# Kernel tuning notes

Measured on AMD Instinct MI355X. Metric: run time of the kernel, lower is better.

The kernel has to match this reference:

```python
import jax, jax.numpy as jnp
import numpy as np
import math

RES = 1024
HEADS = 16
HEAD_RES = RES // HEADS
B, S = 2, 2048


def setup_inputs() -> dict:
    key = jax.random.key(0)
    kx, kq, kk, kv = jax.random.split(key, 4)
    scale = 1.0 / math.sqrt(RES)
    return {
        "x": jax.random.normal(kx, (B, S, RES), dtype=jnp.float32),
        "Wq": jax.random.normal(kq, (RES, RES), dtype=jnp.float32) * scale,
        "Wk": jax.random.normal(kk, (RES, RES), dtype=jnp.float32) * scale,
        "Wv": jax.random.normal(kv, (RES, RES), dtype=jnp.float32) * scale,
    }


def reference(x, Wq, Wk, Wv):
    batch, seq, _ = x.shape
    # projections (torch Linear without bias: x @ W.T; here W stored as [in, out])
    def split_heads(t):
        return t.reshape(batch, seq, HEADS, HEAD_RES).transpose(0, 2, 1, 3)  # [B,H,S,D]
    q = split_heads(x @ Wq)
    k = split_heads(x @ Wk)
    v = split_heads(x @ Wv)
    scores = jnp.einsum("bhsd,bhtd->bhst", q, k) / math.sqrt(HEAD_RES)
    attn = jax.nn.softmax(scores, axis=-1)
    out = jnp.einsum("bhst,bhtd->bhsd", attn, v)  # [B,H,S,D]
    return out.transpose(0, 2, 1, 3).reshape(batch, seq, RES)
```

## Files before the change

### kernel.cpp

```cpp
#include <hip/hip_runtime.h>

typedef _Float16 f16;
typedef _Float16 half8 __attribute__((ext_vector_type(8)));
typedef float f32x4 __attribute__((ext_vector_type(4)));
typedef unsigned int u32x4 __attribute__((ext_vector_type(4)));

#define RES 1024
#define NH 16
#define HD 64
#define BATCH 2
#define SEQ 2048
#define M_ROWS (BATCH * SEQ)

__device__ __forceinline__ void gload_lds16(const void* g, void* l) {
  __builtin_amdgcn_global_load_lds(
      (const __attribute__((address_space(1))) unsigned int*)g,
      (__attribute__((address_space(3))) unsigned int*)l, 16, 0, 0);
}

__device__ __forceinline__ unsigned pk16(float a, float b) {
  auto h = __builtin_amdgcn_cvt_pkrtz(a, b);
  return __builtin_bit_cast(unsigned, h);
}

__device__ __forceinline__ void swap32(unsigned a, unsigned b, unsigned& x, unsigned& y) {
#if __has_builtin(__builtin_amdgcn_permlane32_swap)
  auto t = __builtin_amdgcn_permlane32_swap(a, b, false, false);
  x = (unsigned)t[0];
  y = (unsigned)t[1];
#else
  unsigned ax = __shfl_xor(a, 32), bx = __shfl_xor(b, 32);
  int hi = (threadIdx.x & 63) >> 5;
  x = hi ? bx : a;
  y = hi ? b : ax;
#endif
}

__device__ __forceinline__ void swap16(unsigned a, unsigned b, unsigned& x, unsigned& y) {
#if __has_builtin(__builtin_amdgcn_permlane16_swap)
  auto t = __builtin_amdgcn_permlane16_swap(a, b, false, false);
  x = (unsigned)t[0];
  y = (unsigned)t[1];
#else
  unsigned ax = __shfl_xor(a, 16), bx = __shfl_xor(b, 16);
  int q1 = ((threadIdx.x & 63) >> 4) & 1;
  x = q1 ? bx : a;
  y = q1 ? b : ax;
#endif
}

__global__ __launch_bounds__(256) void xconv_kernel(const float* __restrict__ x,
                                                    f16* __restrict__ xh) {
  int idx = blockIdx.x * 256 + threadIdx.x;
  const float4* xv = (const float4*)x;
  float4 a = xv[idx * 2];
  float4 b = xv[idx * 2 + 1];
  half8 h;
  h[0] = (f16)a.x; h[1] = (f16)a.y; h[2] = (f16)a.z; h[3] = (f16)a.w;
  h[4] = (f16)b.x; h[5] = (f16)b.y; h[6] = (f16)b.z; h[7] = (f16)b.w;
  ((half8*)xh)[idx] = h;
}

__global__ __launch_bounds__(1024) void wtrans_kernel(const float* __restrict__ Wq,
                                                      const float* __restrict__ Wk,
                                                      const float* __restrict__ Wv,
                                                      f16* __restrict__ Wt) {
  const float* W = blockIdx.z == 0 ? Wq : (blockIdx.z == 1 ? Wk : Wv);
  f16* Wo = Wt + (size_t)blockIdx.z * RES * RES;
  __shared__ float tile[32][33];
  int n = blockIdx.x * 32 + threadIdx.x;
  int k = blockIdx.y * 32 + threadIdx.y;
  tile[threadIdx.y][threadIdx.x] = W[(size_t)k * RES + n];
  __syncthreads();
  int ko = blockIdx.y * 32 + threadIdx.x;
  int no = blockIdx.x * 32 + threadIdx.y;
  Wo[(size_t)no * RES + ko] = (f16)tile[threadIdx.x][threadIdx.y];
}

__global__ __launch_bounds__(256) void proj_gemm_kernel(const f16* __restrict__ xh,
                                                        const f16* __restrict__ Wt,
                                                        f16* __restrict__ Qh,
                                                        f16* __restrict__ Kh,
                                                        f16* __restrict__ Vt) {
  int flat = blockIdx.x;
  int swz = (flat & 7) * 96 + (flat >> 3);
  int mb = swz & 31;
  int rest = swz >> 5;
  int nb = rest & 7;
  int proj = rest >> 3;
  const f16* Bt = Wt + (size_t)proj * RES * RES;
  int m0 = mb * 128;
  int n0 = nb * 128;
  __shared__ alignas(16) f16 Als[2][128 * 32];
  __shared__ alignas(16) f16 Bls[2][128 * 32];
  int t = threadIdx.x, lane = t & 63, w = t >> 6;
  int l15 = lane & 15, quad = lane >> 4;
  int wm = w >> 1, wn = w & 1;

  f32x4 zero = {0.f, 0.f, 0.f, 0.f};
  f32x4 acc[4][4];
#pragma unroll
  for (int mt = 0; mt < 4; mt++)
#pragma unroll
    for (int nt = 0; nt < 4; nt++) acc[mt][nt] = zero;

  auto stageAB = [&](int k0, int pb) {
#pragma unroll
    for (int i = 0; i < 2; i++) {
      int wl = i * 256 + w * 64;
      int linear = wl + lane;
      int row = linear >> 2;
      int kk = (linear & 3) * 8;
      gload_lds16(xh + (size_t)(m0 + row) * RES + k0 + kk, &Als[pb][wl * 8]);
      gload_lds16(Bt + (size_t)(n0 + row) * RES + k0 + kk, &Bls[pb][wl * 8]);
    }
  };

  stageAB(0, 0);

  constexpr int KSTEPS = RES / 32;
  for (int it = 0; it < KSTEPS; ++it) {
    int pb = it & 1;
    __syncthreads();

    half8 af[4], bf[4];
#pragma unroll
    for (int mt = 0; mt < 4; mt++)
      af[mt] = *(const half8*)&Als[pb][(wm * 64 + mt * 16 + l15) * 32 + quad * 8];
#pragma unroll
    for (int nt = 0; nt < 4; nt++)
      bf[nt] = *(const half8*)&Bls[pb][(wn * 64 + nt * 16 + l15) * 32 + quad * 8];

    if (it + 1 < KSTEPS) stageAB((it + 1) * 32, pb ^ 1);

#pragma unroll
    for (int mt = 0; mt < 4; mt++)
#pragma unroll
      for (int nt = 0; nt < 4; nt++)
        acc[mt][nt] = __builtin_amdgcn_mfma_f32_16x16x32_f16(af[mt], bf[nt], acc[mt][nt], 0, 0, 0);
  }

#pragma unroll
  for (int mt = 0; mt < 4; mt++) {
#pragma unroll
    for (int nt = 0; nt < 4; nt++) {
#pragma unroll
      for (int r = 0; r < 4; r++) {
        int row = m0 + wm * 64 + mt * 16 + quad * 4 + r;
        int col = n0 + wn * 64 + nt * 16 + l15;
        f16 v = (f16)acc[mt][nt][r];
        int b = row >> 11, s = row & (SEQ - 1);
        int h = col >> 6, d = col & (HD - 1);
        size_t bh = (size_t)b * NH + h;
        if (proj == 0)
          Qh[(bh * SEQ + s) * HD + d] = v;
        else if (proj == 1)
          Kh[(bh * SEQ + s) * HD + d] = v;
        else
          Vt[(bh * HD + d) * SEQ + s] = v;
      }
    }
  }
}

__global__ __launch_bounds__(128, 3) void flash_kernel(const f16* __restrict__ Qh,
                                                       const f16* __restrict__ Kh,
                                                       const f16* __restrict__ Vt,
                                                       float* __restrict__ out) {
  int L = blockIdx.x;
  int xcd = L & 7, slot = L >> 3;
  int bh = ((slot >> 5) << 3) | xcd;
  int qt = slot & 31;
  int b = bh >> 4, h = bh & 15;
  int tid = threadIdx.x;
  int lane = tid & 63, w = tid >> 6;
  int l15 = lane & 15, quad = lane >> 4;
  int qrow0 = qt * 64 + w * 32;

  __shared__ alignas(16) f16 Kls[64 * 64];
  __shared__ alignas(16) f16 Vls[64 * 64];

  const f16* kbase = Kh + (size_t)bh * SEQ * HD;
  const f16* vbase = Vt + (size_t)bh * HD * SEQ;

  int srow = tid >> 3;
  int schunk = tid & 7;

  const f16* qptr = Qh + ((size_t)bh * SEQ + qrow0 + l15) * HD + quad * 8;
  half8 qf[2][2];
  qf[0][0] = *(const half8*)qptr;
  qf[0][1] = *(const half8*)(qptr + 32);
  qf[1][0] = *(const half8*)(qptr + 16 * HD);
  qf[1][1] = *(const half8*)(qptr + 16 * HD + 32);
#pragma unroll
  for (int q2 = 0; q2 < 2; q2++)
#pragma unroll
    for (int ks = 0; ks < 2; ks++)
#pragma unroll
      for (int j = 0; j < 8; j++) qf[q2][ks][j] *= (f16)0.125f;

  f32x4 zero = {0.f, 0.f, 0.f, 0.f};
  float l_acc[2] = {0.f, 0.f};
  f32x4 o[2][4];
#pragma unroll
  for (int q2 = 0; q2 < 2; q2++)
#pragma unroll
    for (int nt = 0; nt < 4; nt++) o[q2][nt] = zero;

  int swz0 = (quad ^ (l15 & 7)) * 8;
  int swz1 = ((quad + 4) ^ (l15 & 7)) * 8;

  auto stage = [&](int kv0) {
#pragma unroll
    for (int rd = 0; rd < 4; rd++) {
      int row = rd * 16 + srow;
      int pc = schunk ^ (row & 7);
      gload_lds16(kbase + ((size_t)(kv0 + row) << 6) + pc * 8,
                  &Kls[rd * 1024 + w * 512]);
      gload_lds16(vbase + ((size_t)row * SEQ) + kv0 + pc * 8,
                  &Vls[rd * 1024 + w * 512]);
    }
  };

  stage(0);

  for (int kv0 = 0; kv0 < SEQ; kv0 += 64) {
    __syncthreads();

    half8 kf0[4], kf1[4];
#pragma unroll
    for (int tt = 0; tt < 4; tt++) {
      int row = tt * 16 + l15;
      kf0[tt] = *(const half8*)&Kls[row * 64 + swz0];
      kf1[tt] = *(const half8*)&Kls[row * 64 + swz1];
    }

    half8 pa[2][2];
#pragma unroll
    for (int q2 = 0; q2 < 2; q2++) {
      f32x4 sc[4];
#pragma unroll
      for (int tt = 0; tt < 4; tt++) {
        sc[tt] = __builtin_amdgcn_mfma_f32_16x16x32_f16(kf0[tt], qf[q2][0], zero, 0, 0, 0);
        sc[tt] = __builtin_amdgcn_mfma_f32_16x16x32_f16(kf1[tt], qf[q2][1], sc[tt], 0, 0, 0);
      }
      float ps = 0.f;
#pragma unroll
      for (int tt = 0; tt < 4; tt++)
#pragma unroll
        for (int r = 0; r < 4; r++) { sc[tt][r] = __expf(sc[tt][r]); ps += sc[tt][r]; }
      ps += __shfl_xor(ps, 16);
      ps += __shfl_xor(ps, 32);
      l_acc[q2] += ps;

      unsigned wp[4][2];
#pragma unroll
      for (int tt = 0; tt < 4; tt++) {
        wp[tt][0] = pk16(sc[tt][0], sc[tt][1]);
        wp[tt][1] = pk16(sc[tt][2], sc[tt][3]);
      }
#pragma unroll
      for (int ks = 0; ks < 2; ks++) {
        u32x4 pw;
#pragma unroll
        for (int i = 0; i < 2; i++) {
          unsigned a, bb, x, y;
          swap32(wp[2 * ks][i], wp[2 * ks + 1][i], a, bb);
          swap16(a, bb, x, y);
          pw[i] = x;
          pw[2 + i] = y;
        }
        pa[q2][ks] = __builtin_bit_cast(half8, pw);
      }
    }

    half8 vf0[4], vf1[4];
#pragma unroll
    for (int nt = 0; nt < 4; nt++) {
      int row = nt * 16 + l15;
      vf0[nt] = *(const half8*)&Vls[row * 64 + swz0];
      vf1[nt] = *(const half8*)&Vls[row * 64 + swz1];
    }

    __syncthreads();

    if (kv0 + 64 < SEQ) stage(kv0 + 64);

#pragma unroll
    for (int q2 = 0; q2 < 2; q2++)
#pragma unroll
      for (int ks = 0; ks < 2; ks++)
#pragma unroll
        for (int nt = 0; nt < 4; nt++)
          o[q2][nt] = __builtin_amdgcn_mfma_f32_16x16x32_f16(pa[q2][ks], ks ? vf1[nt] : vf0[nt], o[q2][nt], 0, 0, 0);
  }

#pragma unroll
  for (int q2 = 0; q2 < 2; q2++) {
    float linv[4];
#pragma unroll
    for (int r = 0; r < 4; r++) linv[r] = 1.0f / __shfl(l_acc[q2], quad * 4 + r);
#pragma unroll
    for (int nt = 0; nt < 4; nt++) {
#pragma unroll
      for (int r = 0; r < 4; r++) {
        int s = qrow0 + q2 * 16 + quad * 4 + r;
        out[((size_t)b * SEQ + s) * RES + h * HD + nt * 16 + l15] = o[q2][nt][r] * linv[r];
      }
    }
  }
}

extern "C" void kernel_launch(void* const* d_in, const int* in_sizes, int n_in,
                              void* d_out, int out_size, void* d_ws, size_t ws_size,
                              hipStream_t stream) {
  (void)in_sizes; (void)n_in; (void)out_size; (void)ws_size;
  const float* x  = (const float*)d_in[0];
  const float* Wq = (const float*)d_in[1];
  const float* Wk = (const float*)d_in[2];
  const float* Wv = (const float*)d_in[3];
  float* out = (float*)d_out;

  f16* xh = (f16*)d_ws;
  f16* Wt = xh + (size_t)M_ROWS * RES;
  f16* Qh = Wt + (size_t)3 * RES * RES;
  f16* Kh = Qh + (size_t)BATCH * NH * SEQ * HD;
  f16* Vt = Kh + (size_t)BATCH * NH * SEQ * HD;

  xconv_kernel<<<M_ROWS * RES / (256 * 8), 256, 0, stream>>>(x, xh);
  wtrans_kernel<<<dim3(32, 32, 3), dim3(32, 32), 0, stream>>>(Wq, Wk, Wv, Wt);
  proj_gemm_kernel<<<768, 256, 0, stream>>>(xh, Wt, Qh, Kh, Vt);
  flash_kernel<<<1024, 128, 0, stream>>>(Qh, Kh, Vt, out);
}
```

Measured before the change: 185.1 us.

## Triple-buffer projection GEMM loads with explicit vmcnt waits and 3D grid

The projection GEMM moves from double to triple LDS buffering, issuing global-to-LDS loads two K-steps ahead. Explicit s_waitcnt vmcnt counts and raw s_barrier calls with sched barriers replace __syncthreads. The block index swizzle for L2 locality is dropped in favor of a plain 3D grid. More LDS per block may lower occupancy, and losing the swizzle may hurt cache reuse.

```diff
diff --git a/kernel.cpp b/kernel.cpp
--- a/kernel.cpp
+++ b/kernel.cpp
@@ -82,17 +82,12 @@
                                                         f16* __restrict__ Qh,
                                                         f16* __restrict__ Kh,
                                                         f16* __restrict__ Vt) {
-  int flat = blockIdx.x;
-  int swz = (flat & 7) * 96 + (flat >> 3);
-  int mb = swz & 31;
-  int rest = swz >> 5;
-  int nb = rest & 7;
-  int proj = rest >> 3;
+  int proj = blockIdx.z;
   const f16* Bt = Wt + (size_t)proj * RES * RES;
-  int m0 = mb * 128;
-  int n0 = nb * 128;
-  __shared__ alignas(16) f16 Als[2][128 * 32];
-  __shared__ alignas(16) f16 Bls[2][128 * 32];
+  int m0 = blockIdx.x * 128;
+  int n0 = blockIdx.y * 128;
+  __shared__ alignas(16) f16 Als[3][128 * 32];
+  __shared__ alignas(16) f16 Bls[3][128 * 32];
   int t = threadIdx.x, lane = t & 63, w = t >> 6;
   int l15 = lane & 15, quad = lane >> 4;
   int wm = w >> 1, wn = w & 1;
@@ -116,12 +111,23 @@
     }
   };
 
+  constexpr int KSTEPS = RES / 32;
   stageAB(0, 0);
-
-  constexpr int KSTEPS = RES / 32;
+  stageAB(32, 1);
+
   for (int it = 0; it < KSTEPS; ++it) {
-    int pb = it & 1;
-    __syncthreads();
+    int pb = it % 3;
+    if (it + 2 < KSTEPS) {
+      stageAB((it + 2) * 32, (it + 2) % 3);
+      asm volatile("s_waitcnt vmcnt(8)" ::: "memory");
+    } else if (it + 1 < KSTEPS) {
+      asm volatile("s_waitcnt vmcnt(4)" ::: "memory");
+    } else {
+      asm volatile("s_waitcnt vmcnt(0)" ::: "memory");
+    }
+    __builtin_amdgcn_sched_barrier(0);
+    __builtin_amdgcn_s_barrier();
+    __builtin_amdgcn_sched_barrier(0);
 
     half8 af[4], bf[4];
 #pragma unroll
@@ -131,13 +137,15 @@
     for (int nt = 0; nt < 4; nt++)
       bf[nt] = *(const half8*)&Bls[pb][(wn * 64 + nt * 16 + l15) * 32 + quad * 8];
 
-    if (it + 1 < KSTEPS) stageAB((it + 1) * 32, pb ^ 1);
-
 #pragma unroll
     for (int mt = 0; mt < 4; mt++)
 #pragma unroll
       for (int nt = 0; nt < 4; nt++)
         acc[mt][nt] = __builtin_amdgcn_mfma_f32_16x16x32_f16(af[mt], bf[nt], acc[mt][nt], 0, 0, 0);
+
+    __builtin_amdgcn_sched_barrier(0);
+    __builtin_amdgcn_s_barrier();
+    __builtin_amdgcn_sched_barrier(0);
   }
 
 #pragma unroll
@@ -329,6 +337,6 @@
 
   xconv_kernel<<<M_ROWS * RES / (256 * 8), 256, 0, stream>>>(x, xh);
   wtrans_kernel<<<dim3(32, 32, 3), dim3(32, 32), 0, stream>>>(Wq, Wk, Wv, Wt);
-  proj_gemm_kernel<<<768, 256, 0, stream>>>(xh, Wt, Qh, Kh, Vt);
+  proj_gemm_kernel<<<dim3(M_ROWS / 128, RES / 128, 3), 256, 0, stream>>>(xh, Wt, Qh, Kh, Vt);
   flash_kernel<<<1024, 128, 0, stream>>>(Qh, Kh, Vt, out);
 }
```

After: 170.0 us. 8.2% less time.
